# Kernel optimization log

Measured on AMD Instinct MI355X. Metric: run time of the kernel, lower is better.

Reference implementation:

```python
import jax, jax.numpy as jnp
import numpy as np
import math

B, N, T, F_IN, F_OUT = 4, 512, 128, 64, 64


def setup_inputs() -> dict:
    key = jax.random.key(0)
    k1, k2, k3 = jax.random.split(key, 3)
    x = jax.random.normal(k1, (B, N, T, F_IN), dtype=jnp.float32)
    adj = jax.random.uniform(k2, (N, N), dtype=jnp.float32)
    theta_w = jax.random.normal(k3, (F_OUT, F_IN), dtype=jnp.float32) * (1.0 / math.sqrt(F_IN))
    return {"x": x, "sym_norm_Adj_matrix": adj, "Theta_w": theta_w}


def reference(x, sym_norm_Adj_matrix, Theta_w):
    b, n, t, f_in = x.shape
    inv_sqrt_f = 1.0 / math.sqrt(f_in)
    # (B, N, T, F) -> (B*T, N, F)
    xt = jnp.transpose(x, (0, 2, 1, 3)).reshape(b * t, n, f_in)
    # attention scores per (batch*time): (BT, N, N)
    score = jnp.einsum('gnf,gmf->gnm', xt, xt) * inv_sqrt_f
    score = jax.nn.softmax(score, axis=-1) * inv_sqrt_f  # second /sqrt(F_in) in forward
    # post-softmax multiplicative adjacency masking, then graph conv matmul
    masked = sym_norm_Adj_matrix[None, :, :] * score      # (BT, N, N)
    agg = jnp.einsum('gnm,gmf->gnf', masked, xt)          # (BT, N, F_in)
    out = jax.nn.relu(agg @ Theta_w.T)                    # (BT, N, F_out)
    # (B, T, N, F_out) -> (B, N, T, F_out)
    return jnp.transpose(out.reshape(b, t, n, -1), (0, 2, 1, 3))
```

## Files before the change

### kernel.cpp

```cpp
#include <hip/hip_runtime.h>
#include <math.h>

#define B_   4
#define N_   512
#define T_   128
#define F_   64
#define QT   128
#define NSTR (T_*F_)
#define RS   144

typedef __attribute__((ext_vector_type(8))) short  s8v;
typedef __attribute__((ext_vector_type(4))) float  f4v;

union F8 { s8v v; unsigned u[4]; uint2 u2[2]; };

__device__ __forceinline__ int swz(int row, int col) {
    return row*RS + ((((col>>3) ^ (row>>3)) & 7) << 4) + ((col & 7) << 1);
}

__device__ __forceinline__ unsigned cvt_pk(float lo, float hi) {
    unsigned r;
    asm("v_cvt_pk_bf16_f32 %0, %1, %2" : "=v"(r) : "v"(lo), "v"(hi));
    return r;
}

#define EXPK 0.18033688f

__global__ __launch_bounds__(256, 3)
void sgcn_mfma5_kernel(const float* __restrict__ x,
                       const float* __restrict__ adj,
                       const float* __restrict__ theta,
                       float* __restrict__ out)
{
    __shared__ char ldsbuf[4*64*RS];

    const int tid  = threadIdx.x;
    const int lane = tid & 63;
    const int w    = tid >> 6;
    const int c15  = lane & 15;
    const int g4   = lane >> 4;

    const int g  = blockIdx.y;
    const int b  = g >> 7;
    const int t  = g & 127;
    const int q0 = blockIdx.x*QT + 32*w;

    const float* xg = x + (size_t)b*N_*NSTR + (size_t)t*F_;

    F8 qf[2][2];
    #pragma unroll
    for (int qt = 0; qt < 2; ++qt)
      #pragma unroll
      for (int kk = 0; kk < 2; ++kk) {
        const float* qp = xg + (size_t)(q0 + 16*qt + c15)*NSTR + 32*kk + 8*g4;
        float4 a = *(const float4*)qp;
        float4 c = *(const float4*)(qp + 4);
        qf[qt][kk].u[0] = cvt_pk(a.x, a.y);
        qf[qt][kk].u[1] = cvt_pk(a.z, a.w);
        qf[qt][kk].u[2] = cvt_pk(c.x, c.y);
        qf[qt][kk].u[3] = cvt_pk(c.z, c.w);
      }

    f4v  Oacc[4][2];
    float l_acc[2] = {0.f, 0.f};
    #pragma unroll
    for (int ft = 0; ft < 4; ++ft)
      #pragma unroll
      for (int qt = 0; qt < 2; ++qt) Oacc[ft][qt] = (f4v)0.f;

    const int nrow = tid >> 4;

    auto stage = [&](char* Xr, char* Xc, const float4* xvv) {
        #pragma unroll
        for (int it = 0; it < 4; ++it) {
            int n = nrow + 16*it;
            unsigned p0 = cvt_pk(xvv[it].x, xvv[it].y);
            unsigned p1 = cvt_pk(xvv[it].z, xvv[it].w);
            *(uint2*)(Xr + swz(n, 4*c15)) = make_uint2(p0, p1);

            unsigned t0 = (unsigned)__shfl_xor((int)p0, 16);
            unsigned t1 = (unsigned)__shfl_xor((int)p1, 16);
            unsigned a  = (g4 & 2) ? p1 : p0;
            unsigned ta = (g4 & 2) ? t1 : t0;
            unsigned bq = (g4 & 2) ? p0 : p1;
            unsigned tb = (g4 & 2) ? t0 : t1;
            unsigned u_mine = (g4 & 1) ? ((ta >> 16) | (a  & 0xffff0000u))
                                       : ((a  & 0xffffu) | (ta << 16));
            unsigned u_oth  = (g4 & 1) ? ((tb >> 16) | (bq & 0xffff0000u))
                                       : ((bq & 0xffffu) | (tb << 16));
            unsigned v2 = (unsigned)__shfl_xor((int)u_oth, 32);
            uint2 wv = (g4 & 2) ? make_uint2(v2, u_mine) : make_uint2(u_mine, v2);
            *(uint2*)(Xc + swz(4*c15 + g4, 32*(it>>1) + 8*w + 4*(it&1))) = wv;
        }
    };

    float4 xv[4];
    #pragma unroll
    for (int it = 0; it < 4; ++it)
        xv[it] = *(const float4*)(xg + (size_t)(nrow + 16*it)*NSTR + 4*c15);
    stage(ldsbuf, ldsbuf + 64*RS, xv);

    for (int kt = 0; kt < 8; ++kt) {
        __syncthreads();

        char* XrowC = ldsbuf + (size_t)(kt & 1) * (2*64*RS);
        char* XcolC = XrowC + 64*RS;
        char* XrowN = ldsbuf + (size_t)((kt & 1) ^ 1) * (2*64*RS);
        char* XcolN = XrowN + 64*RS;

        if (kt < 7) {
            #pragma unroll
            for (int it = 0; it < 4; ++it)
                xv[it] = *(const float4*)(xg + (size_t)((kt+1)*64 + nrow + 16*it)*NSTR + 4*c15);
        }

        F8 pb[2][2];
        #pragma unroll
        for (int mt = 0; mt < 4; ++mt) {
            float4 av[2];
            #pragma unroll
            for (int qt = 0; qt < 2; ++qt)
                av[qt] = *(const float4*)(adj + (size_t)(q0 + 16*qt + c15)*N_ + kt*64 + 16*mt + 4*g4);

            F8 af0, af1;
            af0.v = *(const s8v*)(XrowC + swz(16*mt + c15, 8*g4));
            af1.v = *(const s8v*)(XrowC + swz(16*mt + c15, 32 + 8*g4));

            #pragma unroll
            for (int qt = 0; qt < 2; ++qt) {
                f4v s = (f4v)0.f;
                s = __builtin_amdgcn_mfma_f32_16x16x32_bf16(af0.v, qf[qt][0].v, s, 0, 0, 0);
                s = __builtin_amdgcn_mfma_f32_16x16x32_bf16(af1.v, qf[qt][1].v, s, 0, 0, 0);
                float e0 = __builtin_amdgcn_exp2f(s[0] * EXPK);
                float e1 = __builtin_amdgcn_exp2f(s[1] * EXPK);
                float e2 = __builtin_amdgcn_exp2f(s[2] * EXPK);
                float e3 = __builtin_amdgcn_exp2f(s[3] * EXPK);
                l_acc[qt] += (e0 + e1) + (e2 + e3);
                pb[qt][mt>>1].u[2*(mt&1)  ] = cvt_pk(e0*av[qt].x, e1*av[qt].y);
                pb[qt][mt>>1].u[2*(mt&1)+1] = cvt_pk(e2*av[qt].z, e3*av[qt].w);
            }
        }

        if (kt < 7) stage(XrowN, XcolN, xv);

        #pragma unroll
        for (int kk = 0; kk < 2; ++kk)
          #pragma unroll
          for (int ft = 0; ft < 4; ++ft) {
            F8 vf;
            vf.v = *(const s8v*)(XcolC + swz(16*ft + c15, 32*kk + 8*g4));
            #pragma unroll
            for (int qt = 0; qt < 2; ++qt)
              Oacc[ft][qt] = __builtin_amdgcn_mfma_f32_16x16x32_bf16(vf.v, pb[qt][kk].v, Oacc[ft][qt], 0, 0, 0);
          }
    }

    float inv[2];
    #pragma unroll
    for (int qt = 0; qt < 2; ++qt) {
        float lv = l_acc[qt];
        lv += __shfl_xor(lv, 16);
        lv += __shfl_xor(lv, 32);
        inv[qt] = 0.125f / lv;
    }

    F8 ob[2][2];
    #pragma unroll
    for (int qt = 0; qt < 2; ++qt)
      #pragma unroll
      for (int kk = 0; kk < 2; ++kk) {
        f4v o0 = Oacc[2*kk][qt], o1 = Oacc[2*kk+1][qt];
        ob[qt][kk].u[0] = cvt_pk(o0[0]*inv[qt], o0[1]*inv[qt]);
        ob[qt][kk].u[1] = cvt_pk(o0[2]*inv[qt], o0[3]*inv[qt]);
        ob[qt][kk].u[2] = cvt_pk(o1[0]*inv[qt], o1[1]*inv[qt]);
        ob[qt][kk].u[3] = cvt_pk(o1[2]*inv[qt], o1[3]*inv[qt]);
      }

    F8 tf[4][2];
    #pragma unroll
    for (int ot = 0; ot < 4; ++ot)
      #pragma unroll
      for (int kk = 0; kk < 2; ++kk) {
        const float* tp = theta + (size_t)(16*ot + c15)*F_ + 32*kk + 4*g4;
        float4 a = *(const float4*)tp;
        float4 c = *(const float4*)(tp + 16);
        tf[ot][kk].u[0] = cvt_pk(a.x, a.y);
        tf[ot][kk].u[1] = cvt_pk(a.z, a.w);
        tf[ot][kk].u[2] = cvt_pk(c.x, c.y);
        tf[ot][kk].u[3] = cvt_pk(c.z, c.w);
      }

    f4v R[4][2];
    #pragma unroll
    for (int ot = 0; ot < 4; ++ot)
      #pragma unroll
      for (int qt = 0; qt < 2; ++qt) R[ot][qt] = (f4v)0.f;

    #pragma unroll
    for (int kk = 0; kk < 2; ++kk)
      #pragma unroll
      for (int ot = 0; ot < 4; ++ot)
        #pragma unroll
        for (int qt = 0; qt < 2; ++qt)
          R[ot][qt] = __builtin_amdgcn_mfma_f32_16x16x32_bf16(tf[ot][kk].v, ob[qt][kk].v, R[ot][qt], 0, 0, 0);

    #pragma unroll
    for (int ot = 0; ot < 4; ++ot)
      #pragma unroll
      for (int qt = 0; qt < 2; ++qt) {
        float4 v;
        v.x = fmaxf(R[ot][qt][0], 0.f);
        v.y = fmaxf(R[ot][qt][1], 0.f);
        v.z = fmaxf(R[ot][qt][2], 0.f);
        v.w = fmaxf(R[ot][qt][3], 0.f);
        int q  = q0 + 16*qt + c15;
        int fo = 16*ot + 4*g4;
        *(float4*)(out + ((size_t)(b*N_ + q)*T_ + t)*F_ + fo) = v;
      }
}

extern "C" void kernel_launch(void* const* d_in, const int* in_sizes, int n_in,
                              void* d_out, int out_size, void* d_ws, size_t ws_size,
                              hipStream_t stream) {
    const float* x     = (const float*)d_in[0];
    const float* adj   = (const float*)d_in[1];
    const float* theta = (const float*)d_in[2];
    float* out = (float*)d_out;

    dim3 grid(N_ / QT, B_ * T_);
    sgcn_mfma5_kernel<<<grid, 256, 0, stream>>>(x, adj, theta, out);
}
```

Measured before the change: 107.3 us.

## Use LDS transpose reads to drop duplicate column-major staging of X tile

Replaces the two LDS copies of each X tile (row-major plus a shuffle-built transposed copy) with a single packed layout. The V operand for the aggregation MFMA is now read with ds_read_b64_tr_b16, which transposes in hardware. This removes the cross-lane shuffles and halves LDS writes and footprint. It also moves the next-tile staging after the aggregation MFMAs and adds explicit waitcnt/sched barriers, at the risk of bank conflicts in the unswizzled layout and reduced scheduling freedom.

```diff
diff --git a/kernel.cpp b/kernel.cpp
--- a/kernel.cpp
+++ b/kernel.cpp
@@ -7,16 +7,12 @@
 #define F_   64
 #define QT   128
 #define NSTR (T_*F_)
-#define RS   144
+#define TILE 8192
 
 typedef __attribute__((ext_vector_type(8))) short  s8v;
 typedef __attribute__((ext_vector_type(4))) float  f4v;
 
 union F8 { s8v v; unsigned u[4]; uint2 u2[2]; };
-
-__device__ __forceinline__ int swz(int row, int col) {
-    return row*RS + ((((col>>3) ^ (row>>3)) & 7) << 4) + ((col & 7) << 1);
-}
 
 __device__ __forceinline__ unsigned cvt_pk(float lo, float hi) {
     unsigned r;
@@ -24,15 +20,22 @@
     return r;
 }
 
+template<int OFF>
+__device__ __forceinline__ uint2 tr16(unsigned a) {
+    uint2 d;
+    asm volatile("ds_read_b64_tr_b16 %0, %1 offset:%2" : "=v"(d) : "v"(a), "i"(OFF));
+    return d;
+}
+
 #define EXPK 0.18033688f
 
 __global__ __launch_bounds__(256, 3)
-void sgcn_mfma5_kernel(const float* __restrict__ x,
+void sgcn_mfma6_kernel(const float* __restrict__ x,
                        const float* __restrict__ adj,
                        const float* __restrict__ theta,
                        float* __restrict__ out)
 {
-    __shared__ char ldsbuf[4*64*RS];
+    __shared__ char ldsbuf[2*TILE];
 
     const int tid  = threadIdx.x;
     const int lane = tid & 63;
@@ -69,28 +72,18 @@
       for (int qt = 0; qt < 2; ++qt) Oacc[ft][qt] = (f4v)0.f;
 
     const int nrow = tid >> 4;
-
-    auto stage = [&](char* Xr, char* Xc, const float4* xvv) {
+    const int stoff = (c15>>2)*2048 + w*128 + g4*32 + (c15&3)*8;
+    const int afoff = (g4>>1)*2048 + (c15>>2)*128 + (c15&3)*32 + (g4&1)*16;
+
+    const float* arow0 = adj + (size_t)(q0 +      c15)*N_ + 4*g4;
+    const float* arow1 = adj + (size_t)(q0 + 16 + c15)*N_ + 4*g4;
+
+    auto stage = [&](char* buf, const float4* xvv) {
         #pragma unroll
         for (int it = 0; it < 4; ++it) {
-            int n = nrow + 16*it;
             unsigned p0 = cvt_pk(xvv[it].x, xvv[it].y);
             unsigned p1 = cvt_pk(xvv[it].z, xvv[it].w);
-            *(uint2*)(Xr + swz(n, 4*c15)) = make_uint2(p0, p1);
-
-            unsigned t0 = (unsigned)__shfl_xor((int)p0, 16);
-            unsigned t1 = (unsigned)__shfl_xor((int)p1, 16);
-            unsigned a  = (g4 & 2) ? p1 : p0;
-            unsigned ta = (g4 & 2) ? t1 : t0;
-            unsigned bq = (g4 & 2) ? p0 : p1;
-            unsigned tb = (g4 & 2) ? t0 : t1;
-            unsigned u_mine = (g4 & 1) ? ((ta >> 16) | (a  & 0xffff0000u))
-                                       : ((a  & 0xffffu) | (ta << 16));
-            unsigned u_oth  = (g4 & 1) ? ((tb >> 16) | (bq & 0xffff0000u))
-                                       : ((bq & 0xffffu) | (tb << 16));
-            unsigned v2 = (unsigned)__shfl_xor((int)u_oth, 32);
-            uint2 wv = (g4 & 2) ? make_uint2(v2, u_mine) : make_uint2(u_mine, v2);
-            *(uint2*)(Xc + swz(4*c15 + g4, 32*(it>>1) + 8*w + 4*(it&1))) = wv;
+            *(uint2*)(buf + stoff + it*512) = make_uint2(p0, p1);
         }
     };
 
@@ -98,15 +91,15 @@
     #pragma unroll
     for (int it = 0; it < 4; ++it)
         xv[it] = *(const float4*)(xg + (size_t)(nrow + 16*it)*NSTR + 4*c15);
-    stage(ldsbuf, ldsbuf + 64*RS, xv);
+    stage(ldsbuf, xv);
+
+    const unsigned xb = (unsigned)(uintptr_t)ldsbuf;
 
     for (int kt = 0; kt < 8; ++kt) {
         __syncthreads();
 
-        char* XrowC = ldsbuf + (size_t)(kt & 1) * (2*64*RS);
-        char* XcolC = XrowC + 64*RS;
-        char* XrowN = ldsbuf + (size_t)((kt & 1) ^ 1) * (2*64*RS);
-        char* XcolN = XrowN + 64*RS;
+        char* bufC = ldsbuf + (size_t)(kt & 1) * TILE;
+        char* bufN = ldsbuf + (size_t)((kt & 1) ^ 1) * TILE;
 
         if (kt < 7) {
             #pragma unroll
@@ -117,14 +110,12 @@
         F8 pb[2][2];
         #pragma unroll
         for (int mt = 0; mt < 4; ++mt) {
-            float4 av[2];
-            #pragma unroll
-            for (int qt = 0; qt < 2; ++qt)
-                av[qt] = *(const float4*)(adj + (size_t)(q0 + 16*qt + c15)*N_ + kt*64 + 16*mt + 4*g4);
+            float4 av0 = *(const float4*)(arow0 + kt*64 + 16*mt);
+            float4 av1 = *(const float4*)(arow1 + kt*64 + 16*mt);
 
             F8 af0, af1;
-            af0.v = *(const s8v*)(XrowC + swz(16*mt + c15, 8*g4));
-            af1.v = *(const s8v*)(XrowC + swz(16*mt + c15, 32 + 8*g4));
+            af0.v = *(const s8v*)(bufC + afoff + mt*512);
+            af1.v = *(const s8v*)(bufC + afoff + mt*512 + 4096);
 
             #pragma unroll
             for (int qt = 0; qt < 2; ++qt) {
@@ -136,23 +127,47 @@
                 float e2 = __builtin_amdgcn_exp2f(s[2] * EXPK);
                 float e3 = __builtin_amdgcn_exp2f(s[3] * EXPK);
                 l_acc[qt] += (e0 + e1) + (e2 + e3);
-                pb[qt][mt>>1].u[2*(mt&1)  ] = cvt_pk(e0*av[qt].x, e1*av[qt].y);
-                pb[qt][mt>>1].u[2*(mt&1)+1] = cvt_pk(e2*av[qt].z, e3*av[qt].w);
+                float4 av = qt ? av1 : av0;
+                pb[qt][mt>>1].u[2*(mt&1)  ] = cvt_pk(e0*av.x, e1*av.y);
+                pb[qt][mt>>1].u[2*(mt&1)+1] = cvt_pk(e2*av.z, e3*av.w);
             }
         }
 
-        if (kt < 7) stage(XrowN, XcolN, xv);
-
-        #pragma unroll
-        for (int kk = 0; kk < 2; ++kk)
-          #pragma unroll
-          for (int ft = 0; ft < 4; ++ft) {
-            F8 vf;
-            vf.v = *(const s8v*)(XcolC + swz(16*ft + c15, 32*kk + 8*g4));
-            #pragma unroll
-            for (int qt = 0; qt < 2; ++qt)
-              Oacc[ft][qt] = __builtin_amdgcn_mfma_f32_16x16x32_bf16(vf.v, pb[qt][kk].v, Oacc[ft][qt], 0, 0, 0);
-          }
+        const unsigned va = xb + (unsigned)((kt & 1) * TILE) + (unsigned)(lane * 8);
+        {
+            F8 vf0, vf1, vf2, vf3;
+            vf0.u2[0] = tr16<   0>(va); vf0.u2[1] = tr16< 512>(va);
+            vf1.u2[0] = tr16<2048>(va); vf1.u2[1] = tr16<2560>(va);
+            vf2.u2[0] = tr16<4096>(va); vf2.u2[1] = tr16<4608>(va);
+            vf3.u2[0] = tr16<6144>(va); vf3.u2[1] = tr16<6656>(va);
+            asm volatile("s_waitcnt lgkmcnt(0)" ::: "memory");
+            __builtin_amdgcn_sched_barrier(0);
+            #pragma unroll
+            for (int qt = 0; qt < 2; ++qt) {
+                Oacc[0][qt] = __builtin_amdgcn_mfma_f32_16x16x32_bf16(vf0.v, pb[qt][0].v, Oacc[0][qt], 0, 0, 0);
+                Oacc[1][qt] = __builtin_amdgcn_mfma_f32_16x16x32_bf16(vf1.v, pb[qt][0].v, Oacc[1][qt], 0, 0, 0);
+                Oacc[2][qt] = __builtin_amdgcn_mfma_f32_16x16x32_bf16(vf2.v, pb[qt][0].v, Oacc[2][qt], 0, 0, 0);
+                Oacc[3][qt] = __builtin_amdgcn_mfma_f32_16x16x32_bf16(vf3.v, pb[qt][0].v, Oacc[3][qt], 0, 0, 0);
+            }
+        }
+        {
+            F8 vf0, vf1, vf2, vf3;
+            vf0.u2[0] = tr16<1024>(va); vf0.u2[1] = tr16<1536>(va);
+            vf1.u2[0] = tr16<3072>(va); vf1.u2[1] = tr16<3584>(va);
+            vf2.u2[0] = tr16<5120>(va); vf2.u2[1] = tr16<5632>(va);
+            vf3.u2[0] = tr16<7168>(va); vf3.u2[1] = tr16<7680>(va);
+            asm volatile("s_waitcnt lgkmcnt(0)" ::: "memory");
+            __builtin_amdgcn_sched_barrier(0);
+            #pragma unroll
+            for (int qt = 0; qt < 2; ++qt) {
+                Oacc[0][qt] = __builtin_amdgcn_mfma_f32_16x16x32_bf16(vf0.v, pb[qt][1].v, Oacc[0][qt], 0, 0, 0);
+                Oacc[1][qt] = __builtin_amdgcn_mfma_f32_16x16x32_bf16(vf1.v, pb[qt][1].v, Oacc[1][qt], 0, 0, 0);
+                Oacc[2][qt] = __builtin_amdgcn_mfma_f32_16x16x32_bf16(vf2.v, pb[qt][1].v, Oacc[2][qt], 0, 0, 0);
+                Oacc[3][qt] = __builtin_amdgcn_mfma_f32_16x16x32_bf16(vf3.v, pb[qt][1].v, Oacc[3][qt], 0, 0, 0);
+            }
+        }
+
+        if (kt < 7) stage(bufN, xv);
     }
 
     float inv[2];
@@ -228,5 +243,5 @@
     float* out = (float*)d_out;
 
     dim3 grid(N_ / QT, B_ * T_);
-    sgcn_mfma5_kernel<<<grid, 256, 0, stream>>>(x, adj, theta, out);
-}
+    sgcn_mfma6_kernel<<<grid, 256, 0, stream>>>(x, adj, theta, out);
+}
```

Result: slower. 109.5 us (+2.1%).
